# Performance work log

Measured on AMD Instinct MI355X. Metric: run time of the kernel, lower is better.

The kernel has to match this reference:

```python
import jax, jax.numpy as jnp
import numpy as np

C = 256
CQ = C // 8
B, H, W = 4, 64, 64


def setup_inputs() -> dict:
    key = jax.random.key(0)
    ks = jax.random.split(key, 8)
    x = jax.random.normal(ks[0], (B, C, H, W), dtype=jnp.float32)
    # 1x1 conv weights stored as [out, in]
    wq = jax.random.normal(ks[1], (CQ, C), dtype=jnp.float32) * 0.02
    bq = jnp.zeros((CQ,), dtype=jnp.float32)
    wk = jax.random.normal(ks[2], (CQ, C), dtype=jnp.float32) * 0.02
    bk = jnp.zeros((CQ,), dtype=jnp.float32)
    wv = jax.random.normal(ks[3], (C, C), dtype=jnp.float32) * 0.02
    bv = jnp.zeros((C,), dtype=jnp.float32)
    # gamma initialized nonzero so output depends on attention path
    gamma = jnp.ones((1,), dtype=jnp.float32) * 0.5
    return {"x": x, "wq": wq, "bq": bq, "wk": wk, "bk": bk,
            "wv": wv, "bv": bv, "gamma": gamma}


def reference(x, wq, bq, wk, bk, wv, bv, gamma):
    Bx, Cx, Hx, Wx = x.shape
    N = Hx * Wx
    xf = x.reshape(Bx, Cx, N)                      # [B, C, N]
    q = jnp.einsum('oc,bcn->bon', wq, xf) + bq[None, :, None]  # [B, C/8, N]
    k = jnp.einsum('oc,bcn->bon', wk, xf) + bk[None, :, None]  # [B, C/8, N]
    v = jnp.einsum('oc,bcn->bon', wv, xf) + bv[None, :, None]  # [B, C, N]
    # attn[b,i,j] = softmax_j( sum_d q[b,d,i] * k[b,d,j] )  (no scale factor)
    scores = jnp.einsum('bdi,bdj->bij', q, k)      # [B, N, N]
    attn = jax.nn.softmax(scores, axis=-1)
    # out[b,c,i] = sum_j v[b,c,j] * attn[b,i,j]
    out = jnp.einsum('bcj,bij->bci', v, attn).reshape(Bx, Cx, Hx, Wx)
    return gamma[0] * out + x
```

## Files before the change

### kernel.cpp

```cpp
#include <hip/hip_runtime.h>
#include <math.h>

#define NPIX 4096
#define CH   256
#define CQD  32
#define LOG2E 1.44269504088896340736f

typedef float f32x4 __attribute__((ext_vector_type(4)));
typedef short s16x8 __attribute__((ext_vector_type(8)));

__device__ __forceinline__ unsigned short f2bf(float f) {
  unsigned u = __builtin_bit_cast(unsigned, f);
  return (unsigned short)((u + 0x7FFFu + ((u >> 16) & 1u)) >> 16);
}

__device__ __forceinline__ unsigned cvt_pk_bf16(float a, float b) {
  unsigned d;
  asm("v_cvt_pk_bf16_f32 %0, %1, %2" : "=v"(d) : "v"(a), "v"(b));
  return d;
}

__device__ __forceinline__ f32x4 mfma16(s16x8 a, s16x8 b, f32x4 c) {
  return __builtin_amdgcn_mfma_f32_16x16x32_bf16(a, b, c, 0, 0, 0);
}

__device__ __forceinline__ float fexp2(float x) {
#if __has_builtin(__builtin_amdgcn_exp2f)
  return __builtin_amdgcn_exp2f(x);
#else
  return exp2f(x);
#endif
}

__device__ __forceinline__ float frcp(float x) {
#if __has_builtin(__builtin_amdgcn_rcpf)
  return __builtin_amdgcn_rcpf(x);
#else
  return 1.0f / x;
#endif
}

__global__ __launch_bounds__(256) void wpack_kernel(
    const float* __restrict__ wq, const float* __restrict__ wk,
    const float* __restrict__ wv, unsigned short* __restrict__ Wp)
{
  const int row = blockIdx.x;
  const int c = threadIdx.x;
  float v;
  if (row < 32)      v = wq[row * CH + c] * LOG2E;
  else if (row < 64) v = wk[(row - 32) * CH + c];
  else               v = wv[(row - 64) * CH + c];
  Wp[(size_t)row * CH + c] = f2bf(v);
}

__global__ __launch_bounds__(512, 2) void proj_kernel(
    const float* __restrict__ x, const unsigned short* __restrict__ Wp,
    const float* __restrict__ bq, const float* __restrict__ bk,
    const float* __restrict__ bv,
    unsigned short* __restrict__ Qb, unsigned short* __restrict__ Kb,
    unsigned short* __restrict__ Vb)
{
  __shared__ unsigned short Xs[64][264];

  const int blk = blockIdx.x;
  const int b  = blk >> 6;
  const int p0 = (blk & 63) * 64;
  const int t = threadIdx.x;
  const int w = t >> 6;
  const int lane = t & 63;
  const int g = lane >> 4;
  const int r = lane & 15;

  {
    const int px = t & 63;
    const int cb = (t >> 6) * 4;
    const float* xb = x + (size_t)b * CH * NPIX + p0 + px;
    #pragma unroll
    for (int it = 0; it < 8; ++it) {
      const int c = cb + it * 32;
      const float f0 = xb[(size_t)(c + 0) * NPIX];
      const float f1 = xb[(size_t)(c + 1) * NPIX];
      const float f2 = xb[(size_t)(c + 2) * NPIX];
      const float f3 = xb[(size_t)(c + 3) * NPIX];
      uint2 pk;
      pk.x = cvt_pk_bf16(f0, f1);
      pk.y = cvt_pk_bf16(f2, f3);
      *(uint2*)&Xs[px][c] = pk;
    }
  }
  __syncthreads();

  const int ndd = (w < 4) ? 3 : 2;

  f32x4 acc[3][4];
  #pragma unroll
  for (int dd = 0; dd < 3; ++dd)
    #pragma unroll
    for (int ps = 0; ps < 4; ++ps) { acc[dd][ps][0]=0.f; acc[dd][ps][1]=0.f; acc[dd][ps][2]=0.f; acc[dd][ps][3]=0.f; }

  #pragma unroll
  for (int kt = 0; kt < 8; ++kt) {
    s16x8 xf[4];
    #pragma unroll
    for (int ps = 0; ps < 4; ++ps)
      xf[ps] = *(const s16x8*)&Xs[ps * 16 + r][kt * 32 + g * 8];
    #pragma unroll
    for (int dd = 0; dd < 3; ++dd) {
      if (dd >= ndd) continue;
      const int dt = w + dd * 8;
      const s16x8 wf = *(const s16x8*)&Wp[(size_t)(dt * 16 + r) * CH + kt * 32 + g * 8];
      if (dt < 4) {
        #pragma unroll
        for (int ps = 0; ps < 4; ++ps) acc[dd][ps] = mfma16(xf[ps], wf, acc[dd][ps]);
      } else {
        #pragma unroll
        for (int ps = 0; ps < 4; ++ps) acc[dd][ps] = mfma16(wf, xf[ps], acc[dd][ps]);
      }
    }
  }

  #pragma unroll
  for (int dd = 0; dd < 3; ++dd) {
    if (dd >= ndd) continue;
    const int dt = w + dd * 8;
    if (dt < 4) {
      const int dloc = (dt & 1) * 16;
      float bias = (dt < 2) ? bq[dloc + r] * LOG2E : bk[dloc + r];
      unsigned short* dst = (dt < 2) ? Qb : Kb;
      #pragma unroll
      for (int ps = 0; ps < 4; ++ps)
        #pragma unroll
        for (int e = 0; e < 4; ++e) {
          const int px = p0 + ps * 16 + 4 * g + e;
          dst[((size_t)b * NPIX + px) * CQD + dloc + r] = f2bf(acc[dd][ps][e] + bias);
        }
    } else {
      const int c0v = (dt - 4) * 16;
      const float4 b4 = *(const float4*)&bv[c0v + 4 * g];
      #pragma unroll
      for (int ps = 0; ps < 4; ++ps) {
        const int px = p0 + ps * 16 + r;
        Vb[((size_t)b * CH + c0v + 4 * g + 0) * NPIX + px] = f2bf(acc[dd][ps][0] + b4.x);
        Vb[((size_t)b * CH + c0v + 4 * g + 1) * NPIX + px] = f2bf(acc[dd][ps][1] + b4.y);
        Vb[((size_t)b * CH + c0v + 4 * g + 2) * NPIX + px] = f2bf(acc[dd][ps][2] + b4.z);
        Vb[((size_t)b * CH + c0v + 4 * g + 3) * NPIX + px] = f2bf(acc[dd][ps][3] + b4.w);
      }
    }
  }
}

__global__ __launch_bounds__(256, 2) void attn_kernel(
    const unsigned short* __restrict__ Qb, const unsigned short* __restrict__ Kb,
    const unsigned short* __restrict__ Vb, const float* __restrict__ x,
    const float* __restrict__ gamma, float* __restrict__ out)
{
  __shared__ __align__(16) unsigned short Ps[2][64][72];
  __shared__ float l_s[64];

  const int blk = blockIdx.x;
  const int xcd = blk & 7;
  const int b = xcd >> 1;
  const int split = xcd & 1;
  const int i0 = (blk >> 3) * 64;

  const int tid = threadIdx.x;
  const int w = tid >> 6;
  const int lane = tid & 63;
  const int g = lane >> 4;
  const int r = lane & 15;
  const int c0 = split * 128 + w * 32;

  const unsigned short* __restrict__ Qbase = Qb + (size_t)b * NPIX * CQD;
  const unsigned short* __restrict__ Kbase = Kb + (size_t)b * NPIX * CQD;
  const unsigned short* __restrict__ Vbase = Vb + (size_t)b * CH * NPIX;

  s16x8 qf[4];
  #pragma unroll
  for (int is = 0; is < 4; ++is)
    qf[is] = *(const s16x8*)&Qbase[(size_t)(i0 + is * 16 + r) * CQD + g * 8];

  s16x8 ones;
  #pragma unroll
  for (int j = 0; j < 8; ++j) ones[j] = (short)0x3F80;

  f32x4 o[4][2];
  f32x4 o_l = {0.f, 0.f, 0.f, 0.f};
  #pragma unroll
  for (int is = 0; is < 4; ++is)
    #pragma unroll
    for (int cs = 0; cs < 2; ++cs) { o[is][cs][0]=0.f; o[is][cs][1]=0.f; o[is][cs][2]=0.f; o[is][cs][3]=0.f; }

  s16x8 kf = *(const s16x8*)&Kbase[(size_t)(w * 16 + r) * CQD + g * 8];
  s16x8 vf[2][2];
  #pragma unroll
  for (int cs = 0; cs < 2; ++cs)
    #pragma unroll
    for (int ks = 0; ks < 2; ++ks)
      vf[cs][ks] = *(const s16x8*)&Vbase[(size_t)(c0 + cs * 16 + r) * NPIX + ks * 32 + g * 8];

  #pragma unroll 2
  for (int t = 0; t < 64; ++t) {
    const int cur = t & 1;
    const f32x4 z = {0.f, 0.f, 0.f, 0.f};

    f32x4 s[4];
    #pragma unroll
    for (int is = 0; is < 4; ++is) s[is] = mfma16(kf, qf[is], z);

    const int jn = ((t + 1) & 63) * 64;
    const s16x8 nkf = *(const s16x8*)&Kbase[(size_t)(jn + w * 16 + r) * CQD + g * 8];
    s16x8 nvf[2][2];
    #pragma unroll
    for (int cs = 0; cs < 2; ++cs)
      #pragma unroll
      for (int ks = 0; ks < 2; ++ks)
        nvf[cs][ks] = *(const s16x8*)&Vbase[(size_t)(c0 + cs * 16 + r) * NPIX + jn + ks * 32 + g * 8];

    #pragma unroll
    for (int is = 0; is < 4; ++is) {
      const float p0v = fexp2(s[is][0]);
      const float p1v = fexp2(s[is][1]);
      const float p2v = fexp2(s[is][2]);
      const float p3v = fexp2(s[is][3]);
      uint2 pk;
      pk.x = cvt_pk_bf16(p0v, p1v);
      pk.y = cvt_pk_bf16(p2v, p3v);
      *(uint2*)&Ps[cur][is * 16 + r][w * 16 + 4 * g] = pk;
    }

    __syncthreads();

    #pragma unroll
    for (int is = 0; is < 4; ++is) {
      const s16x8 pb0 = *(const s16x8*)&Ps[cur][is * 16 + r][g * 8];
      const s16x8 pb1 = *(const s16x8*)&Ps[cur][is * 16 + r][32 + g * 8];
      o[is][0] = mfma16(vf[0][0], pb0, o[is][0]);
      o[is][0] = mfma16(vf[0][1], pb1, o[is][0]);
      o[is][1] = mfma16(vf[1][0], pb0, o[is][1]);
      o[is][1] = mfma16(vf[1][1], pb1, o[is][1]);
      if (is == w) {
        o_l = mfma16(ones, pb0, o_l);
        o_l = mfma16(ones, pb1, o_l);
      }
    }

    kf = nkf;
    #pragma unroll
    for (int cs = 0; cs < 2; ++cs)
      #pragma unroll
      for (int ks = 0; ks < 2; ++ks) vf[cs][ks] = nvf[cs][ks];
  }

  if (g == 0) l_s[w * 16 + r] = o_l[0];
  __syncthreads();

  float rl[4];
  #pragma unroll
  for (int is = 0; is < 4; ++is) rl[is] = frcp(l_s[is * 16 + r]);

  const float gam = gamma[0];
  #pragma unroll
  for (int is = 0; is < 4; ++is)
    #pragma unroll
    for (int cs = 0; cs < 2; ++cs)
      #pragma unroll
      for (int e = 0; e < 4; ++e) {
        const int ch = c0 + cs * 16 + 4 * g + e;
        const size_t off = ((size_t)b * CH + ch) * NPIX + i0 + is * 16 + r;
        out[off] = gam * o[is][cs][e] * rl[is] + x[off];
      }
}

extern "C" void kernel_launch(void* const* d_in, const int* in_sizes, int n_in,
                              void* d_out, int out_size, void* d_ws, size_t ws_size,
                              hipStream_t stream) {
  const float* x     = (const float*)d_in[0];
  const float* wq    = (const float*)d_in[1];
  const float* bq    = (const float*)d_in[2];
  const float* wk    = (const float*)d_in[3];
  const float* bk    = (const float*)d_in[4];
  const float* wv    = (const float*)d_in[5];
  const float* bv    = (const float*)d_in[6];
  const float* gamma = (const float*)d_in[7];
  float* out = (float*)d_out;

  unsigned short* Qb = (unsigned short*)d_ws;
  unsigned short* Kb = Qb + (size_t)4 * NPIX * CQD;
  unsigned short* Vb = Kb + (size_t)4 * NPIX * CQD;
  unsigned short* Wp = Vb + (size_t)4 * CH * NPIX;

  hipLaunchKernelGGL(wpack_kernel, dim3(320), dim3(256), 0, stream, wq, wk, wv, Wp);
  hipLaunchKernelGGL(proj_kernel,  dim3(256), dim3(512), 0, stream,
                     x, Wp, bq, bk, bv, Qb, Kb, Vb);
  hipLaunchKernelGGL(attn_kernel,  dim3(512), dim3(256), 0, stream,
                     Qb, Kb, Vb, x, gamma, out);
}
```

Measured before the change: 165.8 us.

## Fuse weight packing into projection, halve pixel tile, swizzle attention P buffer

Removes the separate weight-packing kernel. The projection kernel now reads fp32 weights directly, scales them and converts them to bf16 in registers. The projection tile shrinks from 64 to 32 pixels, so the grid doubles to 512 blocks for better occupancy across CUs. The attention kernel's shared P buffer switches from a padded layout to an XOR-swizzled layout to cut LDS bank conflicts. The costs are redundant weight conversion in every block and more global weight reads per block.

Measured after the change: 175.0 us. 5.5% more time.

```diff
diff --git a/kernel.cpp b/kernel.cpp
--- a/kernel.cpp
+++ b/kernel.cpp
@@ -40,31 +40,19 @@
 #endif
 }
 
-__global__ __launch_bounds__(256) void wpack_kernel(
-    const float* __restrict__ wq, const float* __restrict__ wk,
-    const float* __restrict__ wv, unsigned short* __restrict__ Wp)
-{
-  const int row = blockIdx.x;
-  const int c = threadIdx.x;
-  float v;
-  if (row < 32)      v = wq[row * CH + c] * LOG2E;
-  else if (row < 64) v = wk[(row - 32) * CH + c];
-  else               v = wv[(row - 64) * CH + c];
-  Wp[(size_t)row * CH + c] = f2bf(v);
-}
-
 __global__ __launch_bounds__(512, 2) void proj_kernel(
-    const float* __restrict__ x, const unsigned short* __restrict__ Wp,
-    const float* __restrict__ bq, const float* __restrict__ bk,
-    const float* __restrict__ bv,
+    const float* __restrict__ x,
+    const float* __restrict__ wq, const float* __restrict__ bq,
+    const float* __restrict__ wk, const float* __restrict__ bk,
+    const float* __restrict__ wv, const float* __restrict__ bv,
     unsigned short* __restrict__ Qb, unsigned short* __restrict__ Kb,
     unsigned short* __restrict__ Vb)
 {
-  __shared__ unsigned short Xs[64][264];
+  __shared__ unsigned short Xs[32][264];
 
   const int blk = blockIdx.x;
-  const int b  = blk >> 6;
-  const int p0 = (blk & 63) * 64;
+  const int b  = blk >> 7;
+  const int p0 = (blk & 127) * 32;
   const int t = threadIdx.x;
   const int w = t >> 6;
   const int lane = t & 63;
@@ -72,12 +60,12 @@
   const int r = lane & 15;
 
   {
-    const int px = t & 63;
-    const int cb = (t >> 6) * 4;
+    const int px = t & 31;
+    const int cb = (t >> 5) * 4;
     const float* xb = x + (size_t)b * CH * NPIX + p0 + px;
     #pragma unroll
-    for (int it = 0; it < 8; ++it) {
-      const int c = cb + it * 32;
+    for (int it = 0; it < 4; ++it) {
+      const int c = cb + it * 64;
       const float f0 = xb[(size_t)(c + 0) * NPIX];
       const float f1 = xb[(size_t)(c + 1) * NPIX];
       const float f2 = xb[(size_t)(c + 2) * NPIX];
@@ -92,29 +80,45 @@
 
   const int ndd = (w < 4) ? 3 : 2;
 
-  f32x4 acc[3][4];
+  const float* wrow[3];
+  float wscale[3];
+  #pragma unroll
+  for (int dd = 0; dd < 3; ++dd) {
+    const int dt = w + dd * 8;
+    if (dt < 2)      { wrow[dd] = wq + (size_t)(dt * 16 + r) * CH;       wscale[dd] = LOG2E; }
+    else if (dt < 4) { wrow[dd] = wk + (size_t)((dt - 2) * 16 + r) * CH; wscale[dd] = 1.0f; }
+    else             { wrow[dd] = wv + (size_t)((dt - 4) * 16 + r) * CH; wscale[dd] = 1.0f; }
+  }
+
+  f32x4 acc[3][2];
   #pragma unroll
   for (int dd = 0; dd < 3; ++dd)
     #pragma unroll
-    for (int ps = 0; ps < 4; ++ps) { acc[dd][ps][0]=0.f; acc[dd][ps][1]=0.f; acc[dd][ps][2]=0.f; acc[dd][ps][3]=0.f; }
+    for (int ps = 0; ps < 2; ++ps) { acc[dd][ps][0]=0.f; acc[dd][ps][1]=0.f; acc[dd][ps][2]=0.f; acc[dd][ps][3]=0.f; }
 
   #pragma unroll
   for (int kt = 0; kt < 8; ++kt) {
-    s16x8 xf[4];
-    #pragma unroll
-    for (int ps = 0; ps < 4; ++ps)
-      xf[ps] = *(const s16x8*)&Xs[ps * 16 + r][kt * 32 + g * 8];
+    const s16x8 xf0 = *(const s16x8*)&Xs[     r][kt * 32 + g * 8];
+    const s16x8 xf1 = *(const s16x8*)&Xs[16 + r][kt * 32 + g * 8];
     #pragma unroll
     for (int dd = 0; dd < 3; ++dd) {
       if (dd >= ndd) continue;
       const int dt = w + dd * 8;
-      const s16x8 wf = *(const s16x8*)&Wp[(size_t)(dt * 16 + r) * CH + kt * 32 + g * 8];
+      const float4 wa = *(const float4*)&wrow[dd][kt * 32 + g * 8];
+      const float4 wb = *(const float4*)&wrow[dd][kt * 32 + g * 8 + 4];
+      const float s = wscale[dd];
+      uint4 wu;
+      wu.x = cvt_pk_bf16(wa.x * s, wa.y * s);
+      wu.y = cvt_pk_bf16(wa.z * s, wa.w * s);
+      wu.z = cvt_pk_bf16(wb.x * s, wb.y * s);
+      wu.w = cvt_pk_bf16(wb.z * s, wb.w * s);
+      const s16x8 wf = __builtin_bit_cast(s16x8, wu);
       if (dt < 4) {
-        #pragma unroll
-        for (int ps = 0; ps < 4; ++ps) acc[dd][ps] = mfma16(xf[ps], wf, acc[dd][ps]);
+        acc[dd][0] = mfma16(xf0, wf, acc[dd][0]);
+        acc[dd][1] = mfma16(xf1, wf, acc[dd][1]);
       } else {
-        #pragma unroll
-        for (int ps = 0; ps < 4; ++ps) acc[dd][ps] = mfma16(wf, xf[ps], acc[dd][ps]);
+        acc[dd][0] = mfma16(wf, xf0, acc[dd][0]);
+        acc[dd][1] = mfma16(wf, xf1, acc[dd][1]);
       }
     }
   }
@@ -125,10 +129,10 @@
     const int dt = w + dd * 8;
     if (dt < 4) {
       const int dloc = (dt & 1) * 16;
-      float bias = (dt < 2) ? bq[dloc + r] * LOG2E : bk[dloc + r];
+      const float bias = (dt < 2) ? bq[dloc + r] * LOG2E : bk[dloc + r];
       unsigned short* dst = (dt < 2) ? Qb : Kb;
       #pragma unroll
-      for (int ps = 0; ps < 4; ++ps)
+      for (int ps = 0; ps < 2; ++ps)
         #pragma unroll
         for (int e = 0; e < 4; ++e) {
           const int px = p0 + ps * 16 + 4 * g + e;
@@ -138,7 +142,7 @@
       const int c0v = (dt - 4) * 16;
       const float4 b4 = *(const float4*)&bv[c0v + 4 * g];
       #pragma unroll
-      for (int ps = 0; ps < 4; ++ps) {
+      for (int ps = 0; ps < 2; ++ps) {
         const int px = p0 + ps * 16 + r;
         Vb[((size_t)b * CH + c0v + 4 * g + 0) * NPIX + px] = f2bf(acc[dd][ps][0] + b4.x);
         Vb[((size_t)b * CH + c0v + 4 * g + 1) * NPIX + px] = f2bf(acc[dd][ps][1] + b4.y);
@@ -154,7 +158,7 @@
     const unsigned short* __restrict__ Vb, const float* __restrict__ x,
     const float* __restrict__ gamma, float* __restrict__ out)
 {
-  __shared__ __align__(16) unsigned short Ps[2][64][72];
+  __shared__ __align__(16) unsigned char PsRaw[2][64 * 128];
   __shared__ float l_s[64];
 
   const int blk = blockIdx.x;
@@ -169,6 +173,7 @@
   const int g = lane >> 4;
   const int r = lane & 15;
   const int c0 = split * 128 + w * 32;
+  const int xr = (r & 7) << 4;
 
   const unsigned short* __restrict__ Qbase = Qb + (size_t)b * NPIX * CQD;
   const unsigned short* __restrict__ Kbase = Kb + (size_t)b * NPIX * CQD;
@@ -225,15 +230,16 @@
       uint2 pk;
       pk.x = cvt_pk_bf16(p0v, p1v);
       pk.y = cvt_pk_bf16(p2v, p3v);
-      *(uint2*)&Ps[cur][is * 16 + r][w * 16 + 4 * g] = pk;
+      *(uint2*)&PsRaw[cur][(16 * is + r) * 128 + ((32 * w + 8 * g) ^ xr)] = pk;
     }
 
     __syncthreads();
 
     #pragma unroll
     for (int is = 0; is < 4; ++is) {
-      const s16x8 pb0 = *(const s16x8*)&Ps[cur][is * 16 + r][g * 8];
-      const s16x8 pb1 = *(const s16x8*)&Ps[cur][is * 16 + r][32 + g * 8];
+      const unsigned char* pr = &PsRaw[cur][(16 * is + r) * 128];
+      const s16x8 pb0 = *(const s16x8*)(pr + ((16 * g) ^ xr));
+      const s16x8 pb1 = *(const s16x8*)(pr + ((64 + 16 * g) ^ xr));
       o[is][0] = mfma16(vf[0][0], pb0, o[is][0]);
       o[is][0] = mfma16(vf[0][1], pb1, o[is][0]);
       o[is][1] = mfma16(vf[1][0], pb0, o[is][1]);
@@ -287,11 +293,9 @@
   unsigned short* Qb = (unsigned short*)d_ws;
   unsigned short* Kb = Qb + (size_t)4 * NPIX * CQD;
   unsigned short* Vb = Kb + (size_t)4 * NPIX * CQD;
-  unsigned short* Wp = Vb + (size_t)4 * CH * NPIX;
-
-  hipLaunchKernelGGL(wpack_kernel, dim3(320), dim3(256), 0, stream, wq, wk, wv, Wp);
-  hipLaunchKernelGGL(proj_kernel,  dim3(256), dim3(512), 0, stream,
-                     x, Wp, bq, bk, bv, Qb, Kb, Vb);
-  hipLaunchKernelGGL(attn_kernel,  dim3(512), dim3(256), 0, stream,
+
+  hipLaunchKernelGGL(proj_kernel, dim3(512), dim3(512), 0, stream,
+                     x, wq, bq, wk, bk, wv, bv, Qb, Kb, Vb);
+  hipLaunchKernelGGL(attn_kernel, dim3(512), dim3(256), 0, stream,
                      Qb, Kb, Vb, x, gamma, out);
 }
```
